# Optimization experiments

Measured on AMD Instinct MI355X. Metric: run time of the kernel, lower is better.

The kernel has to match this reference:

```python
import jax, jax.numpy as jnp
import numpy as np

B, S, N, H, NH = 2, 2048, 1024, 1024, 16
D = H // NH  # head dim = 64


def setup_inputs() -> dict:
    key = jax.random.key(0)
    ks = jax.random.split(key, 7)
    scale = 1.0 / np.sqrt(H)
    return {
        "token_q": jax.random.normal(ks[0], (B, S, H), dtype=jnp.float32),
        "block_kv": jax.random.normal(ks[1], (B, N, H), dtype=jnp.float32),
        "block_ends": jnp.sort(jax.random.randint(ks[2], (N,), 0, S, dtype=jnp.int32)),
        "Wq": jax.random.normal(ks[3], (H, H), dtype=jnp.float32) * scale,
        "Wk": jax.random.normal(ks[4], (H, H), dtype=jnp.float32) * scale,
        "Wv": jax.random.normal(ks[5], (H, H), dtype=jnp.float32) * scale,
        "Wo": jax.random.normal(ks[6], (H, H), dtype=jnp.float32) * scale,
    }


def reference(token_q, block_kv, block_ends, Wq, Wk, Wv, Wo):
    # nn.Linear: y = x @ W.T (no bias)
    q = (token_q @ Wq.T).reshape(B, S, NH, D).transpose(0, 2, 1, 3)   # [B,h,S,d]
    k = (block_kv @ Wk.T).reshape(B, N, NH, D).transpose(0, 2, 1, 3)  # [B,h,N,d]
    v = (block_kv @ Wv.T).reshape(B, N, NH, D).transpose(0, 2, 1, 3)  # [B,h,N,d]

    attn = jnp.einsum("bhsd,bhnd->bhsn", q, k) / jnp.sqrt(jnp.float32(D))

    # strict_causal mask: block is visible iff its end position <= query index t
    t_idx = jnp.arange(S, dtype=block_ends.dtype)[:, None]           # [S,1]
    mask = block_ends[None, :] <= t_idx                               # [S,N]
    neg = jnp.finfo(attn.dtype).min
    attn = jnp.where(mask[None, None, :, :], attn, neg)

    attn = jax.nn.softmax(attn, axis=-1)
    out = jnp.einsum("bhsn,bhnd->bhsd", attn, v)                      # [B,h,S,d]
    out = out.transpose(0, 2, 1, 3).reshape(B, S, H)
    return out @ Wo.T
```

## Files before the change

kernel.cpp:

```cpp
#include <hip/hip_runtime.h>
#include <float.h>
#include <stdint.h>

#define B_  2
#define S_  2048
#define N_  1024
#define H_  1024
#define NH_ 16
#define K_  1024

typedef __attribute__((ext_vector_type(8))) short bf16x8;
typedef __attribute__((ext_vector_type(4))) float f32x4;

typedef __attribute__((address_space(3))) uint32_t lds_u32;
typedef __attribute__((address_space(1))) uint32_t glb_u32;

__device__ __forceinline__ void gload16(void* l, const void* g) {
    __builtin_amdgcn_global_load_lds((const glb_u32*)g, (lds_u32*)l, 16, 0, 0);
}

__device__ __forceinline__ ushort f2bf(float f) {
    uint32_t u = __float_as_uint(f);
    u = (u + 0x7fffu + ((u >> 16) & 1u)) >> 16;
    return (ushort)u;
}

#if __has_builtin(__builtin_amdgcn_cvt_pk_bf16_f32)
typedef __attribute__((ext_vector_type(2))) __bf16 bfp2;
__device__ __forceinline__ uint pk2(float a, float b) {
    bfp2 v = __builtin_amdgcn_cvt_pk_bf16_f32(a, b);
    return __builtin_bit_cast(uint, v);
}
#else
__device__ __forceinline__ uint pk2(float a, float b) {
    return (uint)f2bf(a) | ((uint)f2bf(b) << 16);
}
#endif

__device__ __forceinline__ float fexp2(float x) {
#if __has_builtin(__builtin_amdgcn_exp2f)
    return __builtin_amdgcn_exp2f(x);
#else
    return exp2f(x);
#endif
}

#define SC2 0.180336880f

__global__ __launch_bounds__(256) void prep_kernel(const float* __restrict__ tq,
        const float* __restrict__ kv, const float* __restrict__ wq,
        const float* __restrict__ wk, const float* __restrict__ wv,
        const float* __restrict__ wo, const int* __restrict__ ends,
        ushort* __restrict__ dst, int* __restrict__ cnt)
{
    int blk = blockIdx.x;
    if (blk >= 5120) {
        int t = (blk - 5120) * 256 + threadIdx.x;
        if (t < S_) {
            int lo = 0, hi = N_;
            while (lo < hi) { int mid = (lo + hi) >> 1; if (ends[mid] <= t) lo = mid + 1; else hi = mid; }
            cnt[t] = lo;
        }
        return;
    }
    const float* src; size_t base;
    if (blk < 2048)      { src = tq; base = 0;       }
    else if (blk < 3072) { src = kv; base = 4194304; blk -= 2048; }
    else if (blk < 3584) { src = wq; base = 6291456; blk -= 3072; }
    else if (blk < 4096) { src = wk; base = 7340032; blk -= 3584; }
    else if (blk < 4608) { src = wv; base = 8388608; blk -= 4096; }
    else                 { src = wo; base = 9437184; blk -= 4608; }
    size_t i = (size_t)blk * 2048 + threadIdx.x * 8;
    float4 a = *(const float4*)(src + i);
    float4 b = *(const float4*)(src + i + 4);
    uint4 o;
    o.x = pk2(a.x, a.y); o.y = pk2(a.z, a.w);
    o.z = pk2(b.x, b.y); o.w = pk2(b.z, b.w);
    *(uint4*)(dst + base + i) = o;
}

__global__ __launch_bounds__(256) void vmean_kernel(const ushort* __restrict__ Vt,
                                                    float* __restrict__ Vm)
{
    int row = blockIdx.x * 4 + (threadIdx.x >> 6);
    int lane = threadIdx.x & 63;
    const ushort* p = Vt + (size_t)row * N_ + lane * 16;
    uint4 a = *(const uint4*)p;
    uint4 b = *(const uint4*)(p + 8);
    uint u[8] = {a.x, a.y, a.z, a.w, b.x, b.y, b.z, b.w};
    float s = 0.f;
#pragma unroll
    for (int j = 0; j < 8; ++j) {
        s += __uint_as_float(u[j] << 16);
        s += __uint_as_float(u[j] & 0xffff0000u);
    }
#pragma unroll
    for (int off = 1; off < 64; off <<= 1) s += __shfl_xor(s, off);
    if (lane == 0) Vm[row] = s * (1.f / 1024.f);
}

__global__ __launch_bounds__(512) void gemm_all(int mode,
        const ushort* __restrict__ qx, const ushort* __restrict__ kvx,
        const ushort* __restrict__ wq, const ushort* __restrict__ wk,
        const ushort* __restrict__ wv, const ushort* __restrict__ wo,
        ushort* __restrict__ Qp, ushort* __restrict__ Kp,
        ushort* __restrict__ VtG, const ushort* __restrict__ AO,
        float* __restrict__ outF)
{
    __shared__ __align__(16) ushort smem[17408];
    ushort* Xs = smem;
    ushort* Ws = smem + 8192;

    const ushort* X; const ushort* W; void* Yp; int kind; float scale = 1.f;
    int bm, bn;
    if (mode == 1) {
        X = AO; W = wo; Yp = outF; kind = 1;
        bm = (blockIdx.x >> 3) * 128; bn = (blockIdx.x & 7) * 128;
    } else {
        int idx = blockIdx.x;
        if (idx < 256)      { X = qx;  W = wq; Yp = Qp;  kind = 0; scale = SC2;
                              bm = (idx >> 3) * 128; bn = (idx & 7) * 128; }
        else if (idx < 384) { int j = idx - 256; X = kvx; W = wk; Yp = Kp; kind = 0;
                              bm = (j >> 3) * 128; bn = (j & 7) * 128; }
        else                { int j = idx - 384; X = kvx; W = wv; Yp = VtG; kind = 2;
                              bm = (j >> 3) * 128; bn = (j & 7) * 128; }
    }

    const int tid = threadIdx.x;
    const int lane = tid & 63, w = tid >> 6;
    const int wy = w >> 1, wx = w & 1;
    const int c = lane & 15, g = lane >> 4;

    f32x4 acc[2][4] = {};

    for (int kt = 0; kt < 16; ++kt) {
        const int k0 = kt * 64;
#pragma unroll
        for (int j = 0; j < 2; ++j) {
            int u = w * 128 + j * 64 + lane;
            int row = u >> 3, gs = (u & 7) ^ (row & 7);
            gload16(Xs + (w * 128 + j * 64) * 8, X + (size_t)(bm + row) * K_ + k0 + gs * 8);
            gload16(Ws + (w * 128 + j * 64) * 8, W + (size_t)(bn + row) * K_ + k0 + gs * 8);
        }
        __syncthreads();
#pragma unroll
        for (int ks = 0; ks < 2; ++ks) {
            bf16x8 af[2], bfr[4];
#pragma unroll
            for (int mi = 0; mi < 2; ++mi) {
                int row = wy * 32 + mi * 16 + c;
                int s = ks * 4 + g;
                af[mi] = *(const bf16x8*)(Xs + (row * 8 + (s ^ (row & 7))) * 8);
            }
#pragma unroll
            for (int ni = 0; ni < 4; ++ni) {
                int row = wx * 64 + ni * 16 + c;
                int s = ks * 4 + g;
                bfr[ni] = *(const bf16x8*)(Ws + (row * 8 + (s ^ (row & 7))) * 8);
            }
#pragma unroll
            for (int mi = 0; mi < 2; ++mi)
#pragma unroll
                for (int ni = 0; ni < 4; ++ni)
                    acc[mi][ni] = __builtin_amdgcn_mfma_f32_16x16x32_bf16(af[mi], bfr[ni], acc[mi][ni], 0, 0, 0);
        }
        __syncthreads();
    }

    if (kind == 0) {
        ushort* Y = (ushort*)Yp;
#pragma unroll
        for (int mi = 0; mi < 2; ++mi)
#pragma unroll
            for (int ni = 0; ni < 4; ++ni)
#pragma unroll
                for (int r = 0; r < 4; ++r) {
                    int row = bm + wy * 32 + mi * 16 + g * 4 + r;
                    int col = bn + wx * 64 + ni * 16 + c;
                    Y[(size_t)row * 1024 + col] = f2bf(acc[mi][ni][r] * scale);
                }
    } else if (kind == 1) {
        float* Y = (float*)Yp;
#pragma unroll
        for (int mi = 0; mi < 2; ++mi)
#pragma unroll
            for (int ni = 0; ni < 4; ++ni)
#pragma unroll
                for (int r = 0; r < 4; ++r) {
                    int row = bm + wy * 32 + mi * 16 + g * 4 + r;
                    int col = bn + wx * 64 + ni * 16 + c;
                    Y[(size_t)row * 1024 + col] = acc[mi][ni][r];
                }
    } else {
        ushort* T = smem;
#pragma unroll
        for (int mi = 0; mi < 2; ++mi)
#pragma unroll
            for (int ni = 0; ni < 4; ++ni) {
                ushort4 v4;
                v4.x = f2bf(acc[mi][ni][0]); v4.y = f2bf(acc[mi][ni][1]);
                v4.z = f2bf(acc[mi][ni][2]); v4.w = f2bf(acc[mi][ni][3]);
                *(ushort4*)&T[(wx * 64 + ni * 16 + c) * 136 + wy * 32 + mi * 16 + g * 4] = v4;
            }
        __syncthreads();
        ushort* Vt = (ushort*)Yp;
        int b = bm >> 10;
        int rid = tid >> 2, quad = tid & 3;
        int n_c = bn + rid;
        int h = n_c >> 6, d = n_c & 63;
        int m0 = quad * 32;
        ushort* dst = Vt + (size_t)((b * NH_ + h) * 64 + d) * N_ + (bm & (N_ - 1)) + m0;
#pragma unroll
        for (int jj = 0; jj < 4; ++jj)
            *(uint4*)(dst + jj * 8) = *(const uint4*)&T[rid * 136 + m0 + jj * 8];
    }
}

__global__ __launch_bounds__(256) void attn_mfma(const ushort* __restrict__ Qp,
                                                 const ushort* __restrict__ Kp,
                                                 const ushort* __restrict__ VtG,
                                                 const int* __restrict__ cnt,
                                                 const float* __restrict__ Vm,
                                                 ushort* __restrict__ AO)
{
    __shared__ __align__(16) ushort Qs[64 * 64];
    __shared__ __align__(16) ushort Ks[64 * 64];
    __shared__ __align__(16) ushort Vs[64 * 64];
    __shared__ __align__(16) ushort Ps[64][72];

    const int id = blockIdx.x;
    const int b = id & 1, h = (id >> 1) & 15, t0 = (id >> 5) << 6;
    const int tid = threadIdx.x, lane = tid & 63, w = tid >> 6;
    const int c = lane & 15, g = lane >> 4;

    {
        int u0 = (w * 2) * 64 + lane;
        int row0 = u0 >> 3, gs0 = (u0 & 7) ^ (row0 & 7);
        gload16(Qs + (w * 2) * 512, Qp + (size_t)(b * S_ + t0 + row0) * H_ + h * 64 + gs0 * 8);
        int u1 = (w * 2 + 1) * 64 + lane;
        int row1 = u1 >> 3, gs1 = (u1 & 7) ^ (row1 & 7);
        gload16(Qs + (w * 2 + 1) * 512, Qp + (size_t)(b * S_ + t0 + row1) * H_ + h * 64 + gs1 * 8);
    }
    const int cntv = cnt[t0 + w * 16 + c];
    const int cnt_min = cnt[t0];
    const int ntmax = (cnt[t0 + 63] + 63) >> 6;

    const int u0 = (w * 2) * 64 + lane, row0 = u0 >> 3, gs0 = (u0 & 7) ^ (row0 & 7);
    const int u1 = (w * 2 + 1) * 64 + lane, row1 = u1 >> 3, gs1 = (u1 & 7) ^ (row1 & 7);
    const ushort* kp0 = Kp + (size_t)(b * N_ + row0) * H_ + h * 64 + gs0 * 8;
    const ushort* kp1 = Kp + (size_t)(b * N_ + row1) * H_ + h * 64 + gs1 * 8;
    const ushort* vp0 = VtG + (size_t)((b * NH_ + h) * 64 + row0) * N_ + gs0 * 8;
    const ushort* vp1 = VtG + (size_t)((b * NH_ + h) * 64 + row1) * N_ + gs1 * 8;

    float l_run = 0.f;
    f32x4 o[4] = {};

    __syncthreads();
    bf16x8 bq[2];
#pragma unroll
    for (int ks = 0; ks < 2; ++ks) {
        int row = w * 16 + c;
        int s = ks * 4 + g;
        bq[ks] = *(const bf16x8*)(Qs + (row * 8 + (s ^ (row & 7))) * 8);
    }

    for (int nt = 0; nt < ntmax; ++nt) {
        gload16(Ks + (w * 2) * 512, kp0 + (size_t)nt * 64 * H_);
        gload16(Ks + (w * 2 + 1) * 512, kp1 + (size_t)nt * 64 * H_);
        gload16(Vs + (w * 2) * 512, vp0 + nt * 64);
        gload16(Vs + (w * 2 + 1) * 512, vp1 + nt * 64);
        __syncthreads();

        f32x4 st[4] = {};
#pragma unroll
        for (int ntile = 0; ntile < 4; ++ntile)
#pragma unroll
            for (int ks = 0; ks < 2; ++ks) {
                int row = ntile * 16 + c;
                int s = ks * 4 + g;
                bf16x8 ak = *(const bf16x8*)(Ks + (row * 8 + (s ^ (row & 7))) * 8);
                st[ntile] = __builtin_amdgcn_mfma_f32_16x16x32_bf16(ak, bq[ks], st[ntile], 0, 0, 0);
            }

        const bool full = ((nt + 1) << 6) <= cnt_min;
        float lsum = 0.f;
        if (full) {
#pragma unroll
            for (int ntile = 0; ntile < 4; ++ntile) {
                float p0 = fexp2(st[ntile][0]);
                float p1 = fexp2(st[ntile][1]);
                float p2 = fexp2(st[ntile][2]);
                float p3 = fexp2(st[ntile][3]);
                lsum += (p0 + p1) + (p2 + p3);
                uint2 pw; pw.x = pk2(p0, p1); pw.y = pk2(p2, p3);
                *(uint2*)&Ps[w * 16 + c][ntile * 16 + g * 4] = pw;
            }
        } else {
            const int base = (nt << 6) + g * 4 - cntv;
#pragma unroll
            for (int ntile = 0; ntile < 4; ++ntile) {
                float p0 = (base + ntile * 16 + 0 >= 0) ? 0.f : fexp2(st[ntile][0]);
                float p1 = (base + ntile * 16 + 1 >= 0) ? 0.f : fexp2(st[ntile][1]);
                float p2 = (base + ntile * 16 + 2 >= 0) ? 0.f : fexp2(st[ntile][2]);
                float p3 = (base + ntile * 16 + 3 >= 0) ? 0.f : fexp2(st[ntile][3]);
                lsum += (p0 + p1) + (p2 + p3);
                uint2 pw; pw.x = pk2(p0, p1); pw.y = pk2(p2, p3);
                *(uint2*)&Ps[w * 16 + c][ntile * 16 + g * 4] = pw;
            }
        }
        lsum += __shfl_xor(lsum, 16);
        lsum += __shfl_xor(lsum, 32);
        l_run += lsum;

        bf16x8 ap[2];
#pragma unroll
        for (int ks = 0; ks < 2; ++ks)
            ap[ks] = *(const bf16x8*)&Ps[w * 16 + c][ks * 32 + g * 8];
#pragma unroll
        for (int dt = 0; dt < 4; ++dt) {
#pragma unroll
            for (int ks = 0; ks < 2; ++ks) {
                int row = dt * 16 + c;
                int s = ks * 4 + g;
                bf16x8 bv = *(const bf16x8*)(Vs + (row * 8 + (s ^ (row & 7))) * 8);
                o[dt] = __builtin_amdgcn_mfma_f32_16x16x32_bf16(ap[ks], bv, o[dt], 0, 0, 0);
            }
        }
        __syncthreads();
    }

    float invl = 1.f / l_run;
    float lr[4]; int cq[4];
#pragma unroll
    for (int r = 0; r < 4; ++r) {
        lr[r] = __shfl(invl, g * 4 + r);
        cq[r] = cnt[t0 + w * 16 + g * 4 + r];
    }
#pragma unroll
    for (int dt = 0; dt < 4; ++dt)
#pragma unroll
        for (int r = 0; r < 4; ++r) {
            int q = t0 + w * 16 + g * 4 + r;
            float val = o[dt][r] * lr[r];
            if (cq[r] == 0) val = Vm[((b * NH_ + h) << 6) + dt * 16 + c];
            AO[(size_t)(b * S_ + q) * H_ + h * 64 + dt * 16 + c] = f2bf(val);
        }
}

extern "C" void kernel_launch(void* const* d_in, const int* in_sizes, int n_in,
                              void* d_out, int out_size, void* d_ws, size_t ws_size,
                              hipStream_t stream) {
    const float* token_q    = (const float*)d_in[0];
    const float* block_kv   = (const float*)d_in[1];
    const int*   block_ends = (const int*)d_in[2];
    const float* Wq = (const float*)d_in[3];
    const float* Wk = (const float*)d_in[4];
    const float* Wv = (const float*)d_in[5];
    const float* Wo = (const float*)d_in[6];
    float* out = (float*)d_out;

    ushort* ws  = (ushort*)d_ws;
    ushort* qx  = ws;
    ushort* kvx = ws + (size_t)4 * 1024 * 1024;
    ushort* wqb = ws + (size_t)6 * 1024 * 1024;
    ushort* wkb = ws + (size_t)7 * 1024 * 1024;
    ushort* wvb = ws + (size_t)8 * 1024 * 1024;
    ushort* wob = ws + (size_t)9 * 1024 * 1024;
    ushort* Qp  = ws + (size_t)10 * 1024 * 1024;
    ushort* Kp  = ws + (size_t)14 * 1024 * 1024;
    ushort* VtG = ws + (size_t)16 * 1024 * 1024;
    int*    cnt = (int*)(ws + (size_t)18 * 1024 * 1024);
    float*  Vm  = (float*)(ws + (size_t)18 * 1024 * 1024 + 4096);

    prep_kernel<<<5128, 256, 0, stream>>>(token_q, block_kv, Wq, Wk, Wv, Wo,
                                          block_ends, ws, cnt);
    gemm_all<<<512, 512, 0, stream>>>(0, qx, kvx, wqb, wkb, wvb, wob,
                                      Qp, Kp, VtG, nullptr, nullptr);
    vmean_kernel<<<512, 256, 0, stream>>>(VtG, Vm);
    attn_mfma<<<1024, 256, 0, stream>>>(Qp, Kp, VtG, cnt, Vm, Qp);
    gemm_all<<<256, 512, 0, stream>>>(1, qx, kvx, wqb, wkb, wvb, wob,
                                      Qp, Kp, VtG, Qp, out);
}
```

Measured before the change: 161.4 us.

## Fuse V-mean into GEMM epilogue and double attention query tile with balanced ordering

The separate vmean kernel is removed. The V-projection epilogue now accumulates per-column sums through atomics into a buffer that prep_kernel zeroes first. The attention kernel now processes 128 queries per block instead of 64, so each loaded K/V tile is reused across two MFMA query subtiles. Query blocks are ordered to pair light and heavy causal tiles. The change saves one launch and halves K/V traffic per query, in exchange for more registers, larger LDS, fewer blocks (512) and float atomics.

```diff
diff --git a/kernel.cpp b/kernel.cpp
--- a/kernel.cpp
+++ b/kernel.cpp
@@ -51,10 +51,16 @@
         const float* __restrict__ kv, const float* __restrict__ wq,
         const float* __restrict__ wk, const float* __restrict__ wv,
         const float* __restrict__ wo, const int* __restrict__ ends,
-        ushort* __restrict__ dst, int* __restrict__ cnt)
+        ushort* __restrict__ dst, int* __restrict__ cnt, float* __restrict__ Vm)
 {
     int blk = blockIdx.x;
     if (blk >= 5120) {
+        if (blk == 5128) {
+            float4 z = make_float4(0.f, 0.f, 0.f, 0.f);
+            *(float4*)(Vm + threadIdx.x * 8) = z;
+            *(float4*)(Vm + threadIdx.x * 8 + 4) = z;
+            return;
+        }
         int t = (blk - 5120) * 256 + threadIdx.x;
         if (t < S_) {
             int lo = 0, hi = N_;
@@ -79,33 +85,13 @@
     *(uint4*)(dst + base + i) = o;
 }
 
-__global__ __launch_bounds__(256) void vmean_kernel(const ushort* __restrict__ Vt,
-                                                    float* __restrict__ Vm)
-{
-    int row = blockIdx.x * 4 + (threadIdx.x >> 6);
-    int lane = threadIdx.x & 63;
-    const ushort* p = Vt + (size_t)row * N_ + lane * 16;
-    uint4 a = *(const uint4*)p;
-    uint4 b = *(const uint4*)(p + 8);
-    uint u[8] = {a.x, a.y, a.z, a.w, b.x, b.y, b.z, b.w};
-    float s = 0.f;
-#pragma unroll
-    for (int j = 0; j < 8; ++j) {
-        s += __uint_as_float(u[j] << 16);
-        s += __uint_as_float(u[j] & 0xffff0000u);
-    }
-#pragma unroll
-    for (int off = 1; off < 64; off <<= 1) s += __shfl_xor(s, off);
-    if (lane == 0) Vm[row] = s * (1.f / 1024.f);
-}
-
 __global__ __launch_bounds__(512) void gemm_all(int mode,
         const ushort* __restrict__ qx, const ushort* __restrict__ kvx,
         const ushort* __restrict__ wq, const ushort* __restrict__ wk,
         const ushort* __restrict__ wv, const ushort* __restrict__ wo,
         ushort* __restrict__ Qp, ushort* __restrict__ Kp,
         ushort* __restrict__ VtG, const ushort* __restrict__ AO,
-        float* __restrict__ outF)
+        float* __restrict__ outF, float* __restrict__ Vm)
 {
     __shared__ __align__(16) ushort smem[17408];
     ushort* Xs = smem;
@@ -210,9 +196,21 @@
         int h = n_c >> 6, d = n_c & 63;
         int m0 = quad * 32;
         ushort* dst = Vt + (size_t)((b * NH_ + h) * 64 + d) * N_ + (bm & (N_ - 1)) + m0;
-#pragma unroll
-        for (int jj = 0; jj < 4; ++jj)
-            *(uint4*)(dst + jj * 8) = *(const uint4*)&T[rid * 136 + m0 + jj * 8];
+        float vsum = 0.f;
+#pragma unroll
+        for (int jj = 0; jj < 4; ++jj) {
+            uint4 tt = *(const uint4*)&T[rid * 136 + m0 + jj * 8];
+            *(uint4*)(dst + jj * 8) = tt;
+            uint uu[4] = {tt.x, tt.y, tt.z, tt.w};
+#pragma unroll
+            for (int q2 = 0; q2 < 4; ++q2) {
+                vsum += __uint_as_float(uu[q2] << 16);
+                vsum += __uint_as_float(uu[q2] & 0xffff0000u);
+            }
+        }
+        vsum += __shfl_xor(vsum, 1);
+        vsum += __shfl_xor(vsum, 2);
+        if (quad == 0) atomicAdd(&Vm[b * 1024 + n_c], vsum);
     }
 }
 
@@ -223,27 +221,29 @@
                                                  const float* __restrict__ Vm,
                                                  ushort* __restrict__ AO)
 {
-    __shared__ __align__(16) ushort Qs[64 * 64];
+    __shared__ __align__(16) ushort Qs[128 * 64];
     __shared__ __align__(16) ushort Ks[64 * 64];
     __shared__ __align__(16) ushort Vs[64 * 64];
-    __shared__ __align__(16) ushort Ps[64][72];
+    __shared__ __align__(16) ushort Ps[128][72];
 
     const int id = blockIdx.x;
-    const int b = id & 1, h = (id >> 1) & 15, t0 = (id >> 5) << 6;
+    const int b = id & 1, h = (id >> 1) & 15;
+    const int tb = id >> 5;
+    const int t0 = (tb < 8 ? tb : 23 - tb) << 7;
     const int tid = threadIdx.x, lane = tid & 63, w = tid >> 6;
     const int c = lane & 15, g = lane >> 4;
 
-    {
-        int u0 = (w * 2) * 64 + lane;
-        int row0 = u0 >> 3, gs0 = (u0 & 7) ^ (row0 & 7);
-        gload16(Qs + (w * 2) * 512, Qp + (size_t)(b * S_ + t0 + row0) * H_ + h * 64 + gs0 * 8);
-        int u1 = (w * 2 + 1) * 64 + lane;
-        int row1 = u1 >> 3, gs1 = (u1 & 7) ^ (row1 & 7);
-        gload16(Qs + (w * 2 + 1) * 512, Qp + (size_t)(b * S_ + t0 + row1) * H_ + h * 64 + gs1 * 8);
-    }
-    const int cntv = cnt[t0 + w * 16 + c];
+#pragma unroll
+    for (int jj = 0; jj < 4; ++jj) {
+        int u = w * 256 + jj * 64 + lane;
+        int row = u >> 3, gs = (u & 7) ^ (row & 7);
+        gload16(Qs + (w * 256 + jj * 64) * 8,
+                Qp + (size_t)(b * S_ + t0 + row) * H_ + h * 64 + gs * 8);
+    }
+    const int cntv0 = cnt[t0 + w * 32 + c];
+    const int cntv1 = cnt[t0 + w * 32 + 16 + c];
     const int cnt_min = cnt[t0];
-    const int ntmax = (cnt[t0 + 63] + 63) >> 6;
+    const int ntmax = (cnt[t0 + 127] + 63) >> 6;
 
     const int u0 = (w * 2) * 64 + lane, row0 = u0 >> 3, gs0 = (u0 & 7) ^ (row0 & 7);
     const int u1 = (w * 2 + 1) * 64 + lane, row1 = u1 >> 3, gs1 = (u1 & 7) ^ (row1 & 7);
@@ -252,16 +252,18 @@
     const ushort* vp0 = VtG + (size_t)((b * NH_ + h) * 64 + row0) * N_ + gs0 * 8;
     const ushort* vp1 = VtG + (size_t)((b * NH_ + h) * 64 + row1) * N_ + gs1 * 8;
 
-    float l_run = 0.f;
-    f32x4 o[4] = {};
+    float l0 = 0.f, l1 = 0.f;
+    f32x4 o0[4] = {}, o1[4] = {};
 
     __syncthreads();
-    bf16x8 bq[2];
+    bf16x8 bq0[2], bq1[2];
 #pragma unroll
     for (int ks = 0; ks < 2; ++ks) {
-        int row = w * 16 + c;
         int s = ks * 4 + g;
-        bq[ks] = *(const bf16x8*)(Qs + (row * 8 + (s ^ (row & 7))) * 8);
+        int ra = w * 32 + c;
+        bq0[ks] = *(const bf16x8*)(Qs + (ra * 8 + (s ^ (ra & 7))) * 8);
+        int rb = w * 32 + 16 + c;
+        bq1[ks] = *(const bf16x8*)(Qs + (rb * 8 + (s ^ (rb & 7))) * 8);
     }
 
     for (int nt = 0; nt < ntmax; ++nt) {
@@ -271,7 +273,7 @@
         gload16(Vs + (w * 2 + 1) * 512, vp1 + nt * 64);
         __syncthreads();
 
-        f32x4 st[4] = {};
+        f32x4 st0[4] = {}, st1[4] = {};
 #pragma unroll
         for (int ntile = 0; ntile < 4; ++ntile)
 #pragma unroll
@@ -279,72 +281,90 @@
                 int row = ntile * 16 + c;
                 int s = ks * 4 + g;
                 bf16x8 ak = *(const bf16x8*)(Ks + (row * 8 + (s ^ (row & 7))) * 8);
-                st[ntile] = __builtin_amdgcn_mfma_f32_16x16x32_bf16(ak, bq[ks], st[ntile], 0, 0, 0);
+                st0[ntile] = __builtin_amdgcn_mfma_f32_16x16x32_bf16(ak, bq0[ks], st0[ntile], 0, 0, 0);
+                st1[ntile] = __builtin_amdgcn_mfma_f32_16x16x32_bf16(ak, bq1[ks], st1[ntile], 0, 0, 0);
             }
 
         const bool full = ((nt + 1) << 6) <= cnt_min;
-        float lsum = 0.f;
+        float lsum0 = 0.f, lsum1 = 0.f;
         if (full) {
 #pragma unroll
             for (int ntile = 0; ntile < 4; ++ntile) {
-                float p0 = fexp2(st[ntile][0]);
-                float p1 = fexp2(st[ntile][1]);
-                float p2 = fexp2(st[ntile][2]);
-                float p3 = fexp2(st[ntile][3]);
-                lsum += (p0 + p1) + (p2 + p3);
-                uint2 pw; pw.x = pk2(p0, p1); pw.y = pk2(p2, p3);
-                *(uint2*)&Ps[w * 16 + c][ntile * 16 + g * 4] = pw;
+                float a0 = fexp2(st0[ntile][0]), a1 = fexp2(st0[ntile][1]);
+                float a2 = fexp2(st0[ntile][2]), a3 = fexp2(st0[ntile][3]);
+                lsum0 += (a0 + a1) + (a2 + a3);
+                uint2 pw; pw.x = pk2(a0, a1); pw.y = pk2(a2, a3);
+                *(uint2*)&Ps[w * 32 + c][ntile * 16 + g * 4] = pw;
+                float b0 = fexp2(st1[ntile][0]), b1 = fexp2(st1[ntile][1]);
+                float b2 = fexp2(st1[ntile][2]), b3 = fexp2(st1[ntile][3]);
+                lsum1 += (b0 + b1) + (b2 + b3);
+                uint2 qw; qw.x = pk2(b0, b1); qw.y = pk2(b2, b3);
+                *(uint2*)&Ps[w * 32 + 16 + c][ntile * 16 + g * 4] = qw;
             }
         } else {
-            const int base = (nt << 6) + g * 4 - cntv;
+            const int base0 = (nt << 6) + g * 4 - cntv0;
+            const int base1 = (nt << 6) + g * 4 - cntv1;
 #pragma unroll
             for (int ntile = 0; ntile < 4; ++ntile) {
-                float p0 = (base + ntile * 16 + 0 >= 0) ? 0.f : fexp2(st[ntile][0]);
-                float p1 = (base + ntile * 16 + 1 >= 0) ? 0.f : fexp2(st[ntile][1]);
-                float p2 = (base + ntile * 16 + 2 >= 0) ? 0.f : fexp2(st[ntile][2]);
-                float p3 = (base + ntile * 16 + 3 >= 0) ? 0.f : fexp2(st[ntile][3]);
-                lsum += (p0 + p1) + (p2 + p3);
-                uint2 pw; pw.x = pk2(p0, p1); pw.y = pk2(p2, p3);
-                *(uint2*)&Ps[w * 16 + c][ntile * 16 + g * 4] = pw;
-            }
-        }
-        lsum += __shfl_xor(lsum, 16);
-        lsum += __shfl_xor(lsum, 32);
-        l_run += lsum;
-
-        bf16x8 ap[2];
-#pragma unroll
-        for (int ks = 0; ks < 2; ++ks)
-            ap[ks] = *(const bf16x8*)&Ps[w * 16 + c][ks * 32 + g * 8];
-#pragma unroll
-        for (int dt = 0; dt < 4; ++dt) {
+                float a0 = (base0 + ntile * 16 + 0 >= 0) ? 0.f : fexp2(st0[ntile][0]);
+                float a1 = (base0 + ntile * 16 + 1 >= 0) ? 0.f : fexp2(st0[ntile][1]);
+                float a2 = (base0 + ntile * 16 + 2 >= 0) ? 0.f : fexp2(st0[ntile][2]);
+                float a3 = (base0 + ntile * 16 + 3 >= 0) ? 0.f : fexp2(st0[ntile][3]);
+                lsum0 += (a0 + a1) + (a2 + a3);
+                uint2 pw; pw.x = pk2(a0, a1); pw.y = pk2(a2, a3);
+                *(uint2*)&Ps[w * 32 + c][ntile * 16 + g * 4] = pw;
+                float b0 = (base1 + ntile * 16 + 0 >= 0) ? 0.f : fexp2(st1[ntile][0]);
+                float b1 = (base1 + ntile * 16 + 1 >= 0) ? 0.f : fexp2(st1[ntile][1]);
+                float b2 = (base1 + ntile * 16 + 2 >= 0) ? 0.f : fexp2(st1[ntile][2]);
+                float b3 = (base1 + ntile * 16 + 3 >= 0) ? 0.f : fexp2(st1[ntile][3]);
+                lsum1 += (b0 + b1) + (b2 + b3);
+                uint2 qw; qw.x = pk2(b0, b1); qw.y = pk2(b2, b3);
+                *(uint2*)&Ps[w * 32 + 16 + c][ntile * 16 + g * 4] = qw;
+            }
+        }
+        lsum0 += __shfl_xor(lsum0, 16); lsum0 += __shfl_xor(lsum0, 32);
+        lsum1 += __shfl_xor(lsum1, 16); lsum1 += __shfl_xor(lsum1, 32);
+        l0 += lsum0; l1 += lsum1;
+
+        bf16x8 ap0[2], ap1[2];
+#pragma unroll
+        for (int ks = 0; ks < 2; ++ks) {
+            ap0[ks] = *(const bf16x8*)&Ps[w * 32 + c][ks * 32 + g * 8];
+            ap1[ks] = *(const bf16x8*)&Ps[w * 32 + 16 + c][ks * 32 + g * 8];
+        }
+#pragma unroll
+        for (int dt = 0; dt < 4; ++dt)
 #pragma unroll
             for (int ks = 0; ks < 2; ++ks) {
                 int row = dt * 16 + c;
                 int s = ks * 4 + g;
                 bf16x8 bv = *(const bf16x8*)(Vs + (row * 8 + (s ^ (row & 7))) * 8);
-                o[dt] = __builtin_amdgcn_mfma_f32_16x16x32_bf16(ap[ks], bv, o[dt], 0, 0, 0);
-            }
-        }
+                o0[dt] = __builtin_amdgcn_mfma_f32_16x16x32_bf16(ap0[ks], bv, o0[dt], 0, 0, 0);
+                o1[dt] = __builtin_amdgcn_mfma_f32_16x16x32_bf16(ap1[ks], bv, o1[dt], 0, 0, 0);
+            }
         __syncthreads();
     }
 
-    float invl = 1.f / l_run;
-    float lr[4]; int cq[4];
-#pragma unroll
-    for (int r = 0; r < 4; ++r) {
-        lr[r] = __shfl(invl, g * 4 + r);
-        cq[r] = cnt[t0 + w * 16 + g * 4 + r];
-    }
-#pragma unroll
-    for (int dt = 0; dt < 4; ++dt)
+#pragma unroll
+    for (int qt = 0; qt < 2; ++qt) {
+        float invl = 1.f / (qt == 0 ? l0 : l1);
+        f32x4* o = (qt == 0 ? o0 : o1);
+        float lr[4]; int cq[4];
 #pragma unroll
         for (int r = 0; r < 4; ++r) {
-            int q = t0 + w * 16 + g * 4 + r;
-            float val = o[dt][r] * lr[r];
-            if (cq[r] == 0) val = Vm[((b * NH_ + h) << 6) + dt * 16 + c];
-            AO[(size_t)(b * S_ + q) * H_ + h * 64 + dt * 16 + c] = f2bf(val);
-        }
+            lr[r] = __shfl(invl, g * 4 + r);
+            cq[r] = cnt[t0 + w * 32 + qt * 16 + g * 4 + r];
+        }
+#pragma unroll
+        for (int dt = 0; dt < 4; ++dt)
+#pragma unroll
+            for (int r = 0; r < 4; ++r) {
+                int q = t0 + w * 32 + qt * 16 + g * 4 + r;
+                float val = o[dt][r] * lr[r];
+                if (cq[r] == 0) val = Vm[b * 1024 + h * 64 + dt * 16 + c] * (1.f / 1024.f);
+                AO[(size_t)(b * S_ + q) * H_ + h * 64 + dt * 16 + c] = f2bf(val);
+            }
+    }
 }
 
 extern "C" void kernel_launch(void* const* d_in, const int* in_sizes, int n_in,
@@ -372,12 +392,11 @@
     int*    cnt = (int*)(ws + (size_t)18 * 1024 * 1024);
     float*  Vm  = (float*)(ws + (size_t)18 * 1024 * 1024 + 4096);
 
-    prep_kernel<<<5128, 256, 0, stream>>>(token_q, block_kv, Wq, Wk, Wv, Wo,
-                                          block_ends, ws, cnt);
+    prep_kernel<<<5129, 256, 0, stream>>>(token_q, block_kv, Wq, Wk, Wv, Wo,
+                                          block_ends, ws, cnt, Vm);
     gemm_all<<<512, 512, 0, stream>>>(0, qx, kvx, wqb, wkb, wvb, wob,
-                                      Qp, Kp, VtG, nullptr, nullptr);
-    vmean_kernel<<<512, 256, 0, stream>>>(VtG, Vm);
-    attn_mfma<<<1024, 256, 0, stream>>>(Qp, Kp, VtG, cnt, Vm, Qp);
+                                      Qp, Kp, VtG, nullptr, nullptr, Vm);
+    attn_mfma<<<512, 256, 0, stream>>>(Qp, Kp, VtG, cnt, Vm, Qp);
     gemm_all<<<256, 512, 0, stream>>>(1, qx, kvx, wqb, wkb, wvb, wob,
-                                      Qp, Kp, VtG, Qp, out);
-}
+                                      Qp, Kp, VtG, Qp, out, Vm);
+}
```

Result: no change. 163.0 us (+1.0%).
